# Kernel tuning notes

Hardware: AMD Instinct MI355X
Metric: run time of the kernel (lower is better)

The kernel has to match this reference:

```python
import jax, jax.numpy as jnp
import numpy as np

KH, KW = 3, 3
SH, SW = 1, 1
IC, OC = 32, 32
M = 4
P = M * M
ITERS = 3
LAM = 1.0
EPS = 1e-8


def _patches(t, kh, kw, sh, sw):
    # t: [B, H, W, ...] -> [B, Ho, Wo, kh, kw, ...] (im2col, matches torch unfold+permute)
    H, W = t.shape[1], t.shape[2]
    Ho = (H - kh) // sh + 1
    Wo = (W - kw) // sw + 1
    i = (jnp.arange(Ho) * sh)[:, None] + jnp.arange(kh)[None, :]  # [Ho,kh]
    j = (jnp.arange(Wo) * sw)[:, None] + jnp.arange(kw)[None, :]  # [Wo,kw]
    tp = t[:, i]            # [B,Ho,kh,W,...]
    tp = tp[:, :, :, j]     # [B,Ho,kh,Wo,kw,...]
    return jnp.moveaxis(tp, 2, 3)  # [B,Ho,Wo,kh,kw,...]


def setup_inputs() -> dict:
    key = jax.random.key(0)
    k1, k2, k3, k4, k5 = jax.random.split(key, 5)
    x = jax.random.normal(k1, (4, 14, 14, IC, M, M), dtype=jnp.float32)
    a = jax.random.uniform(k2, (4, 14, 14, IC), dtype=jnp.float32)
    W = jax.random.uniform(k3, (KH, KW, IC, OC, M, M), dtype=jnp.float32)   # torch.rand init
    beta_u = jax.random.uniform(k4, (1, OC, 1), dtype=jnp.float32)
    beta_a = jax.random.uniform(k5, (1, OC), dtype=jnp.float32)
    return {"x": x, "a": a, "W": W, "beta_u": beta_u, "beta_a": beta_a}


def reference(x, a, W, beta_u, beta_a):
    # im2col patches
    xp = _patches(x, KH, KW, SH, SW)          # [B,Ho,Wo,kh,kw,IC,M,M]
    ap = _patches(a, KH, KW, SH, SW)          # [B,Ho,Wo,kh,kw,IC]
    # pose-transform votes: per (kh,kw,inCap,outCap) 4x4 matmul
    V = jnp.einsum('bhwklcxy,klcoyz->bhwklcoxz', xp, W)
    B, Ho, Wo = V.shape[:3]
    N = KH * KW * IC
    V = V.reshape(B, Ho, Wo, N, OC, P)        # votes
    a_in = ap.reshape(B, Ho, Wo, N)
    bu = beta_u.reshape(OC, 1)
    ba = beta_a.reshape(OC)

    # EM routing (Hinton et al. 2018, fixed inverse temperature)
    R = jnp.full((B, Ho, Wo, N, OC), 1.0 / OC, dtype=V.dtype)
    for it in range(ITERS):
        Ra = R * a_in[..., None]                                  # [B,Ho,Wo,N,OC]
        Rs = Ra.sum(axis=3) + EPS                                 # [B,Ho,Wo,OC]
        mu = jnp.einsum('bhwno,bhwnop->bhwop', Ra, V) / Rs[..., None]
        d = V - mu[:, :, :, None]                                 # [B,Ho,Wo,N,OC,P]
        sig2 = jnp.einsum('bhwno,bhwnop->bhwop', Ra, d * d) / Rs[..., None] + EPS
        cost = (bu + 0.5 * jnp.log(sig2)) * Rs[..., None]         # [B,Ho,Wo,OC,P]
        a_out = jax.nn.sigmoid(LAM * (ba - cost.sum(-1)))         # [B,Ho,Wo,OC]
        if it < ITERS - 1:
            logp = -0.5 * jnp.sum(d * d / sig2[:, :, :, None] + jnp.log(sig2)[:, :, :, None], axis=-1)
            R = jax.nn.softmax(jnp.log(a_out + EPS)[:, :, :, None] + logp, axis=-1)

    pose = mu.reshape(B, Ho, Wo, OC, M, M)
    return pose, a_out
```

## Files before the change

kernel.cpp:

```cpp
#include <hip/hip_runtime.h>


#define NN    288
#define EPSV  1e-8f

template <int CTRL>
__device__ __forceinline__ float dppf(float v) {
  return __int_as_float(__builtin_amdgcn_update_dpp(
      0, __float_as_int(v), CTRL, 0xf, 0xf, true));
}
__device__ __forceinline__ float swz16(float v) {
  return __int_as_float(__builtin_amdgcn_ds_swizzle(__float_as_int(v), 0x401F));
}
__device__ __forceinline__ float red_max32(float v) {
  v = fmaxf(v, dppf<0xB1>(v));
  v = fmaxf(v, dppf<0x4E>(v));
  v = fmaxf(v, dppf<0x141>(v));
  v = fmaxf(v, dppf<0x140>(v));
  v = fmaxf(v, swz16(v));
  return v;
}
__device__ __forceinline__ float red_sum32(float v) {
  v += dppf<0xB1>(v);
  v += dppf<0x4E>(v);
  v += dppf<0x141>(v);
  v += dppf<0x140>(v);
  v += swz16(v);
  return v;
}

__device__ __forceinline__ void compute_votes(const float* __restrict__ Wt,
                                              const float* __restrict__ xp_s,
                                              int n, int o, float* __restrict__ V)
{
  float Wf[16];
  {
    const float* wp = Wt + (((n << 5) + o) << 4);
#pragma unroll
    for (int i = 0; i < 4; ++i) {
      const float4 q = *(const float4*)(wp + (i << 2));
      Wf[i*4+0]=q.x; Wf[i*4+1]=q.y; Wf[i*4+2]=q.z; Wf[i*4+3]=q.w;
    }
  }
  float xv[16];
  {
    const float* xr = xp_s + (n << 4);
#pragma unroll
    for (int i = 0; i < 4; ++i) {
      const float4 q = *(const float4*)(xr + (i << 2));
      xv[i*4+0]=q.x; xv[i*4+1]=q.y; xv[i*4+2]=q.z; xv[i*4+3]=q.w;
    }
  }
#pragma unroll
  for (int xi = 0; xi < 4; ++xi)
#pragma unroll
    for (int z = 0; z < 4; ++z)
      V[xi*4+z] = fmaf(xv[xi*4+0], Wf[z],
                  fmaf(xv[xi*4+1], Wf[4+z],
                  fmaf(xv[xi*4+2], Wf[8+z],
                       xv[xi*4+3]* Wf[12+z])));
}

__global__ __launch_bounds__(512, 4) void caps_em_kernel(
    const float* __restrict__ X, const float* __restrict__ A, const float* __restrict__ Wt,
    const float* __restrict__ Bu, const float* __restrict__ Ba,
    float* __restrict__ Out)
{
  __shared__ float xp_s[NN*16];
  __shared__ float a_s[NN];
  __shared__ float part[8*544];
  __shared__ float prs[8*32];
  __shared__ float mu_t[512];
  __shared__ float isig_t[512];
  __shared__ float lsig_t[512];
  __shared__ float la_s[32];
  __shared__ float slog_s[32];
  __shared__ float aout_s[32];

  const int t    = threadIdx.x;
  const int o    = t & 31;
  const int ng   = t >> 5;
  const int wv   = t >> 6;
  const int lane = t & 63;

  const int pos = blockIdx.x;
  const int b  = pos / 144;
  const int r_ = pos - b*144;
  const int h  = r_ / 12;
  const int w  = r_ - (r_/12)*12;

  for (int i = t; i < 1152; i += 512) {
    const int e   = i << 2;
    const int kl  = e >> 9;
    const int rem = e & 511;
    const int hy = h + kl/3, wx = w + (kl - (kl/3)*3);
    const float4 q = *(const float4*)(X + ((((b*14 + hy)*14 + wx) << 9) + rem));
    *(float4*)(xp_s + (kl << 9) + rem) = q;
  }
  for (int i = t; i < NN; i += 512) {
    const int kl = i >> 5, c = i & 31;
    const int hy = h + kl/3, wx = w + (kl - (kl/3)*3);
    a_s[i] = A[((b*14 + hy)*14 + wx)*32 + c];
  }
  __syncthreads();

  float mu_r[16], isig_r[16];
  float la_r = 0.f, slog_r = 0.f;
#pragma unroll
  for (int p = 0; p < 16; ++p) { mu_r[p] = 0.f; isig_r[p] = 0.f; }

  for (int it = 0; it < 3; ++it) {
    float S1[16], S2[16];
#pragma unroll
    for (int p = 0; p < 16; ++p) { S1[p] = 0.f; S2[p] = 0.f; }
    float rs = 0.f;

#pragma unroll 1
    for (int j = 0; j < 18; ++j) {
      const int n = ng + (j << 4);
      float V[16];
      compute_votes(Wt, xp_s, n, o, V);

      float ra;
      if (it == 0) {
        ra = a_s[n] * (1.0f/32.0f);
      } else {
        float q0 = 0.f, q1 = 0.f, q2 = 0.f, q3 = 0.f;
#pragma unroll
        for (int p = 0; p < 4; ++p) {
          float d;
          d = V[p]      - mu_r[p];      q0 = fmaf(d*d, isig_r[p],      q0);
          d = V[p+4]    - mu_r[p+4];    q1 = fmaf(d*d, isig_r[p+4],    q1);
          d = V[p+8]    - mu_r[p+8];    q2 = fmaf(d*d, isig_r[p+8],    q2);
          d = V[p+12]   - mu_r[p+12];   q3 = fmaf(d*d, isig_r[p+12],   q3);
        }
        const float q = slog_r + ((q0 + q1) + (q2 + q3));
        const float z = la_r - 0.5f*q;
        const float m  = red_max32(z);
        const float ev = __expf(z - m);
        const float s  = red_sum32(ev);
        ra = (ev / s) * a_s[n];
      }
      rs += ra;
#pragma unroll
      for (int p = 0; p < 16; ++p) {
        const float rv = ra * V[p];
        S1[p] += rv;
        S2[p] = fmaf(rv, V[p], S2[p]);
      }
    }

#pragma unroll
    for (int p = 0; p < 16; ++p) {
      S1[p] += __shfl_xor(S1[p], 32);
      S2[p] += __shfl_xor(S2[p], 32);
    }
    rs += __shfl_xor(rs, 32);

    if (lane < 32) {
      float* p1 = part + wv*544 + o*17;
#pragma unroll
      for (int p = 0; p < 16; ++p) p1[p] = S1[p];
      prs[wv*32 + o] = rs;
    }
    __syncthreads();
    {
      const int pi = t >> 5, oo = t & 31;
      float s1 = 0.f, rsum = EPSV;
#pragma unroll
      for (int g = 0; g < 8; ++g) {
        s1   += part[g*544 + oo*17 + pi];
        rsum += prs[(g << 5) + oo];
      }
      mu_t[pi*32 + oo] = s1 / rsum;
    }
    __syncthreads();

    if (lane < 32) {
      float* p2 = part + wv*544 + o*17;
#pragma unroll
      for (int p = 0; p < 16; ++p) p2[p] = S2[p];
    }
    __syncthreads();
    {
      const int pi = t >> 5, oo = t & 31;
      float s2 = 0.f, rsum = EPSV;
#pragma unroll
      for (int g = 0; g < 8; ++g) {
        s2   += part[g*544 + oo*17 + pi];
        rsum += prs[(g << 5) + oo];
      }
      const float mu = mu_t[pi*32 + oo];
      float var = s2 / rsum - mu*mu;
      var = fmaxf(var, 0.f);
      const float sg = var + EPSV;
      isig_t[pi*32 + oo] = 1.0f / sg;
      lsig_t[pi*32 + oo] = __logf(sg);
    }
    __syncthreads();

    if (t < 32) {
      float rsum = EPSV;
#pragma unroll
      for (int g = 0; g < 8; ++g) rsum += prs[(g << 5) + t];
      float slog = 0.f;
#pragma unroll
      for (int p = 0; p < 16; ++p) slog += lsig_t[p*32 + t];
      const float bu = Bu[t];
      const float ba = Ba[t];
      const float cost = rsum * (16.0f*bu + 0.5f*slog);
      const float av = 1.0f / (1.0f + __expf(-(ba - cost)));
      aout_s[t] = av;
      la_s[t]   = __logf(av + EPSV);
      slog_s[t] = slog;
    }
    __syncthreads();

    if (it < 2) {
#pragma unroll
      for (int p = 0; p < 16; ++p) {
        mu_r[p]   = mu_t[p*32 + o];
        isig_r[p] = isig_t[p*32 + o];
      }
      slog_r = slog_s[o];
      la_r   = la_s[o];
    }
  }

  {
    const int oo = t >> 4, pi = t & 15;
    Out[pos*512 + t] = mu_t[pi*32 + oo];
  }
  if (t < 32) Out[294912 + pos*32 + t] = aout_s[t];
}

extern "C" void kernel_launch(void* const* d_in, const int* in_sizes, int n_in,
                              void* d_out, int out_size, void* d_ws, size_t ws_size,
                              hipStream_t stream) {
  (void)in_sizes; (void)n_in; (void)d_ws; (void)ws_size; (void)out_size;
  const float* X  = (const float*)d_in[0];
  const float* A  = (const float*)d_in[1];
  const float* Wt = (const float*)d_in[2];
  const float* Bu = (const float*)d_in[3];
  const float* Ba = (const float*)d_in[4];
  float* Out = (float*)d_out;
  hipLaunchKernelGGL(caps_em_kernel, dim3(576), dim3(512), 0, stream,
                     X, A, Wt, Bu, Ba, Out);
}
```

Baseline: 168.5 us.

## Split EM routing across kernel launches with half-N blocks and global partial sums

Splits each output position's work across two blocks, each handling half of the 288 input capsules. The three EM iterations become separate kernel launches that exchange partial S1/S2/rs sums through a workspace buffer, followed by a final kernel that computes pose and activation. This doubles the grid to 1152 blocks to improve parallelism across CUs. In exchange it adds launch overhead, global-memory round trips, and recomputation of votes and patch loads in every launch.

```diff
diff --git a/kernel.cpp b/kernel.cpp
--- a/kernel.cpp
+++ b/kernel.cpp
@@ -1,8 +1,7 @@
 #include <hip/hip_runtime.h>
 
 
-#define NN    288
-#define EPSV  1e-8f
+#define EPSV 1e-8f
 
 template <int CTRL>
 __device__ __forceinline__ float dppf(float v) {
@@ -30,7 +29,7 @@
 }
 
 __device__ __forceinline__ void compute_votes(const float* __restrict__ Wt,
-                                              const float* __restrict__ xp_s,
+                                              const float* __restrict__ xr,
                                               int n, int o, float* __restrict__ V)
 {
   float Wf[16];
@@ -43,13 +42,10 @@
     }
   }
   float xv[16];
-  {
-    const float* xr = xp_s + (n << 4);
-#pragma unroll
-    for (int i = 0; i < 4; ++i) {
-      const float4 q = *(const float4*)(xr + (i << 2));
-      xv[i*4+0]=q.x; xv[i*4+1]=q.y; xv[i*4+2]=q.z; xv[i*4+3]=q.w;
-    }
+#pragma unroll
+  for (int i = 0; i < 4; ++i) {
+    const float4 q = *(const float4*)(xr + (i << 2));
+    xv[i*4+0]=q.x; xv[i*4+1]=q.y; xv[i*4+2]=q.z; xv[i*4+3]=q.w;
   }
 #pragma unroll
   for (int xi = 0; xi < 4; ++xi)
@@ -61,21 +57,17 @@
                        xv[xi*4+3]* Wf[12+z])));
 }
 
-__global__ __launch_bounds__(512, 4) void caps_em_kernel(
+__global__ __launch_bounds__(512, 4) void caps_stats(
     const float* __restrict__ X, const float* __restrict__ A, const float* __restrict__ Wt,
     const float* __restrict__ Bu, const float* __restrict__ Ba,
-    float* __restrict__ Out)
+    const float* __restrict__ prev, float* __restrict__ cur, int it)
 {
-  __shared__ float xp_s[NN*16];
-  __shared__ float a_s[NN];
+  __shared__ float xp_s[144*16];
+  __shared__ float a_s[144];
   __shared__ float part[8*544];
   __shared__ float prs[8*32];
-  __shared__ float mu_t[512];
-  __shared__ float isig_t[512];
-  __shared__ float lsig_t[512];
-  __shared__ float la_s[32];
-  __shared__ float slog_s[32];
-  __shared__ float aout_s[32];
+  __shared__ float mu_t[512], isig_t[512], lsig_t[512];
+  __shared__ float la_s[32], slog_s[32], rs_s[32];
 
   const int t    = threadIdx.x;
   const int o    = t & 31;
@@ -83,150 +75,191 @@
   const int wv   = t >> 6;
   const int lane = t & 63;
 
-  const int pos = blockIdx.x;
+  const int bid  = blockIdx.x;
+  const int pos  = bid >> 1;
+  const int half = bid & 1;
   const int b  = pos / 144;
   const int r_ = pos - b*144;
   const int h  = r_ / 12;
   const int w  = r_ - (r_/12)*12;
-
-  for (int i = t; i < 1152; i += 512) {
-    const int e   = i << 2;
-    const int kl  = e >> 9;
-    const int rem = e & 511;
+  const int nbase = half * 144;
+
+  for (int i = t; i < 576; i += 512) {
+    const int r  = i >> 2, q4 = i & 3;
+    const int n  = nbase + r;
+    const int kl = n >> 5, c = n & 31;
     const int hy = h + kl/3, wx = w + (kl - (kl/3)*3);
-    const float4 q = *(const float4*)(X + ((((b*14 + hy)*14 + wx) << 9) + rem));
-    *(float4*)(xp_s + (kl << 9) + rem) = q;
-  }
-  for (int i = t; i < NN; i += 512) {
-    const int kl = i >> 5, c = i & 31;
+    const float4 v = *(const float4*)(X + ((((b*14+hy)*14+wx) << 9) + (c << 4) + (q4 << 2)));
+    *(float4*)(xp_s + (r << 4) + (q4 << 2)) = v;
+  }
+  if (t < 144) {
+    const int n  = nbase + t;
+    const int kl = n >> 5, c = n & 31;
     const int hy = h + kl/3, wx = w + (kl - (kl/3)*3);
-    a_s[i] = A[((b*14 + hy)*14 + wx)*32 + c];
-  }
-  __syncthreads();
+    a_s[t] = A[((b*14+hy)*14+wx)*32 + c];
+  }
 
   float mu_r[16], isig_r[16];
   float la_r = 0.f, slog_r = 0.f;
-#pragma unroll
-  for (int p = 0; p < 16; ++p) { mu_r[p] = 0.f; isig_r[p] = 0.f; }
-
-  for (int it = 0; it < 3; ++it) {
-    float S1[16], S2[16];
-#pragma unroll
-    for (int p = 0; p < 16; ++p) { S1[p] = 0.f; S2[p] = 0.f; }
-    float rs = 0.f;
-
-#pragma unroll 1
-    for (int j = 0; j < 18; ++j) {
-      const int n = ng + (j << 4);
-      float V[16];
-      compute_votes(Wt, xp_s, n, o, V);
-
-      float ra;
-      if (it == 0) {
-        ra = a_s[n] * (1.0f/32.0f);
-      } else {
-        float q0 = 0.f, q1 = 0.f, q2 = 0.f, q3 = 0.f;
-#pragma unroll
-        for (int p = 0; p < 4; ++p) {
-          float d;
-          d = V[p]      - mu_r[p];      q0 = fmaf(d*d, isig_r[p],      q0);
-          d = V[p+4]    - mu_r[p+4];    q1 = fmaf(d*d, isig_r[p+4],    q1);
-          d = V[p+8]    - mu_r[p+8];    q2 = fmaf(d*d, isig_r[p+8],    q2);
-          d = V[p+12]   - mu_r[p+12];   q3 = fmaf(d*d, isig_r[p+12],   q3);
-        }
-        const float q = slog_r + ((q0 + q1) + (q2 + q3));
-        const float z = la_r - 0.5f*q;
-        const float m  = red_max32(z);
-        const float ev = __expf(z - m);
-        const float s  = red_sum32(ev);
-        ra = (ev / s) * a_s[n];
-      }
-      rs += ra;
-#pragma unroll
-      for (int p = 0; p < 16; ++p) {
-        const float rv = ra * V[p];
-        S1[p] += rv;
-        S2[p] = fmaf(rv, V[p], S2[p]);
-      }
-    }
-
-#pragma unroll
-    for (int p = 0; p < 16; ++p) {
-      S1[p] += __shfl_xor(S1[p], 32);
-      S2[p] += __shfl_xor(S2[p], 32);
-    }
-    rs += __shfl_xor(rs, 32);
-
-    if (lane < 32) {
-      float* p1 = part + wv*544 + o*17;
-#pragma unroll
-      for (int p = 0; p < 16; ++p) p1[p] = S1[p];
-      prs[wv*32 + o] = rs;
-    }
-    __syncthreads();
+
+  if (it > 0) {
     {
       const int pi = t >> 5, oo = t & 31;
-      float s1 = 0.f, rsum = EPSV;
-#pragma unroll
-      for (int g = 0; g < 8; ++g) {
-        s1   += part[g*544 + oo*17 + pi];
-        rsum += prs[(g << 5) + oo];
-      }
-      mu_t[pi*32 + oo] = s1 / rsum;
-    }
-    __syncthreads();
-
-    if (lane < 32) {
-      float* p2 = part + wv*544 + o*17;
-#pragma unroll
-      for (int p = 0; p < 16; ++p) p2[p] = S2[p];
-    }
-    __syncthreads();
-    {
-      const int pi = t >> 5, oo = t & 31;
-      float s2 = 0.f, rsum = EPSV;
-#pragma unroll
-      for (int g = 0; g < 8; ++g) {
-        s2   += part[g*544 + oo*17 + pi];
-        rsum += prs[(g << 5) + oo];
-      }
-      const float mu = mu_t[pi*32 + oo];
+      const float* h0 = prev + (pos*2+0)*1056;
+      const float* h1 = prev + (pos*2+1)*1056;
+      const int idx = pi*32 + oo;
+      const float s1   = h0[idx]       + h1[idx];
+      const float s2   = h0[512+idx]   + h1[512+idx];
+      const float rsum = h0[1024+oo]   + h1[1024+oo] + EPSV;
+      const float mu = s1 / rsum;
       float var = s2 / rsum - mu*mu;
       var = fmaxf(var, 0.f);
       const float sg = var + EPSV;
-      isig_t[pi*32 + oo] = 1.0f / sg;
-      lsig_t[pi*32 + oo] = __logf(sg);
+      mu_t[idx]   = mu;
+      isig_t[idx] = 1.0f / sg;
+      lsig_t[idx] = __logf(sg);
+      if (pi == 0) rs_s[oo] = rsum;
     }
     __syncthreads();
-
     if (t < 32) {
-      float rsum = EPSV;
-#pragma unroll
-      for (int g = 0; g < 8; ++g) rsum += prs[(g << 5) + t];
       float slog = 0.f;
 #pragma unroll
       for (int p = 0; p < 16; ++p) slog += lsig_t[p*32 + t];
-      const float bu = Bu[t];
-      const float ba = Ba[t];
-      const float cost = rsum * (16.0f*bu + 0.5f*slog);
-      const float av = 1.0f / (1.0f + __expf(-(ba - cost)));
-      aout_s[t] = av;
+      const float cost = rs_s[t] * (16.0f*Bu[t] + 0.5f*slog);
+      const float av = 1.0f / (1.0f + __expf(-(Ba[t] - cost)));
       la_s[t]   = __logf(av + EPSV);
       slog_s[t] = slog;
     }
     __syncthreads();
-
-    if (it < 2) {
-#pragma unroll
-      for (int p = 0; p < 16; ++p) {
-        mu_r[p]   = mu_t[p*32 + o];
-        isig_r[p] = isig_t[p*32 + o];
+#pragma unroll
+    for (int p = 0; p < 16; ++p) { mu_r[p] = mu_t[p*32 + o]; isig_r[p] = isig_t[p*32 + o]; }
+    slog_r = slog_s[o];
+    la_r   = la_s[o];
+  } else {
+#pragma unroll
+    for (int p = 0; p < 16; ++p) { mu_r[p] = 0.f; isig_r[p] = 0.f; }
+    __syncthreads();
+  }
+
+  float S1[16], S2[16];
+#pragma unroll
+  for (int p = 0; p < 16; ++p) { S1[p] = 0.f; S2[p] = 0.f; }
+  float rs = 0.f;
+
+#pragma unroll 1
+  for (int j = 0; j < 9; ++j) {
+    const int nl = ng + (j << 4);
+    const int n  = nbase + nl;
+    float V[16];
+    compute_votes(Wt, xp_s + (nl << 4), n, o, V);
+
+    float ra;
+    if (it == 0) {
+      ra = a_s[nl] * (1.0f/32.0f);
+    } else {
+      float q0 = 0.f, q1 = 0.f, q2 = 0.f, q3 = 0.f;
+#pragma unroll
+      for (int p = 0; p < 4; ++p) {
+        float d;
+        d = V[p]    - mu_r[p];    q0 = fmaf(d*d, isig_r[p],    q0);
+        d = V[p+4]  - mu_r[p+4];  q1 = fmaf(d*d, isig_r[p+4],  q1);
+        d = V[p+8]  - mu_r[p+8];  q2 = fmaf(d*d, isig_r[p+8],  q2);
+        d = V[p+12] - mu_r[p+12]; q3 = fmaf(d*d, isig_r[p+12], q3);
       }
-      slog_r = slog_s[o];
-      la_r   = la_s[o];
-    }
-  }
-
+      const float q = slog_r + ((q0 + q1) + (q2 + q3));
+      const float z = la_r - 0.5f*q;
+      const float m  = red_max32(z);
+      const float ev = __expf(z - m);
+      const float s  = red_sum32(ev);
+      ra = (ev / s) * a_s[nl];
+    }
+    rs += ra;
+#pragma unroll
+    for (int p = 0; p < 16; ++p) {
+      const float rv = ra * V[p];
+      S1[p] += rv;
+      S2[p] = fmaf(rv, V[p], S2[p]);
+    }
+  }
+
+#pragma unroll
+  for (int p = 0; p < 16; ++p) {
+    S1[p] += __shfl_xor(S1[p], 32);
+    S2[p] += __shfl_xor(S2[p], 32);
+  }
+  rs += __shfl_xor(rs, 32);
+
+  float* dst = cur + bid*1056;
+
+  if (lane < 32) {
+    float* p1 = part + wv*544 + o*17;
+#pragma unroll
+    for (int p = 0; p < 16; ++p) p1[p] = S1[p];
+    prs[wv*32 + o] = rs;
+  }
+  __syncthreads();
+  {
+    const int pi = t >> 5, oo = t & 31;
+    float s1 = 0.f;
+#pragma unroll
+    for (int g = 0; g < 8; ++g) s1 += part[g*544 + oo*17 + pi];
+    dst[t] = s1;
+    if (t < 32) {
+      float r = 0.f;
+#pragma unroll
+      for (int g = 0; g < 8; ++g) r += prs[(g << 5) + t];
+      dst[1024 + t] = r;
+    }
+  }
+  __syncthreads();
+
+  if (lane < 32) {
+    float* p2 = part + wv*544 + o*17;
+#pragma unroll
+    for (int p = 0; p < 16; ++p) p2[p] = S2[p];
+  }
+  __syncthreads();
+  {
+    const int pi = t >> 5, oo = t & 31;
+    float s2 = 0.f;
+#pragma unroll
+    for (int g = 0; g < 8; ++g) s2 += part[g*544 + oo*17 + pi];
+    dst[512 + t] = s2;
+  }
+}
+
+__global__ __launch_bounds__(512, 4) void caps_final(
+    const float* __restrict__ prev, const float* __restrict__ Bu,
+    const float* __restrict__ Ba, float* __restrict__ Out)
+{
+  __shared__ float mu_t[512], lsig_t[512], rs_s[32], aout_s[32];
+
+  const int t   = threadIdx.x;
+  const int pos = blockIdx.x;
+  {
+    const int pi = t >> 5, oo = t & 31;
+    const float* h0 = prev + (pos*2+0)*1056;
+    const float* h1 = prev + (pos*2+1)*1056;
+    const int idx = pi*32 + oo;
+    const float s1   = h0[idx]     + h1[idx];
+    const float s2   = h0[512+idx] + h1[512+idx];
+    const float rsum = h0[1024+oo] + h1[1024+oo] + EPSV;
+    const float mu = s1 / rsum;
+    float var = s2 / rsum - mu*mu;
+    var = fmaxf(var, 0.f);
+    mu_t[idx]   = mu;
+    lsig_t[idx] = __logf(var + EPSV);
+    if (pi == 0) rs_s[oo] = rsum;
+  }
+  __syncthreads();
+  if (t < 32) {
+    float slog = 0.f;
+#pragma unroll
+    for (int p = 0; p < 16; ++p) slog += lsig_t[p*32 + t];
+    const float cost = rs_s[t] * (16.0f*Bu[t] + 0.5f*slog);
+    aout_s[t] = 1.0f / (1.0f + __expf(-(Ba[t] - cost)));
+  }
+  __syncthreads();
   {
     const int oo = t >> 4, pi = t & 15;
     Out[pos*512 + t] = mu_t[pi*32 + oo];
@@ -237,13 +270,23 @@
 extern "C" void kernel_launch(void* const* d_in, const int* in_sizes, int n_in,
                               void* d_out, int out_size, void* d_ws, size_t ws_size,
                               hipStream_t stream) {
-  (void)in_sizes; (void)n_in; (void)d_ws; (void)ws_size; (void)out_size;
+  (void)in_sizes; (void)n_in; (void)ws_size; (void)out_size;
   const float* X  = (const float*)d_in[0];
   const float* A  = (const float*)d_in[1];
   const float* Wt = (const float*)d_in[2];
   const float* Bu = (const float*)d_in[3];
   const float* Ba = (const float*)d_in[4];
   float* Out = (float*)d_out;
-  hipLaunchKernelGGL(caps_em_kernel, dim3(576), dim3(512), 0, stream,
-                     X, A, Wt, Bu, Ba, Out);
-}
+
+  float* pa = (float*)d_ws;
+  float* pb = pa + 1152*1056;
+
+  hipLaunchKernelGGL(caps_stats, dim3(1152), dim3(512), 0, stream,
+                     X, A, Wt, Bu, Ba, (const float*)nullptr, pa, 0);
+  hipLaunchKernelGGL(caps_stats, dim3(1152), dim3(512), 0, stream,
+                     X, A, Wt, Bu, Ba, pa, pb, 1);
+  hipLaunchKernelGGL(caps_stats, dim3(1152), dim3(512), 0, stream,
+                     X, A, Wt, Bu, Ba, pb, pa, 2);
+  hipLaunchKernelGGL(caps_final, dim3(576), dim3(512), 0, stream,
+                     pa, Bu, Ba, Out);
+}
```

Result: faster. 162.4 us (-3.6%).
